# Kernel tuning notes

Hardware: AMD Instinct MI355X
Metric: run time of the kernel (lower is better)

Reference implementation:

```python
import jax, jax.numpy as jnp
import numpy as np

ANGULAR_WEIGHT = 0.1
EPS = 1e-07


def nine_d_to_rotmat(nine_d):
    # nine_d: [B, 9] -> special-orthogonal [B, 3, 3] via SVD Procrustes
    mats = nine_d.reshape(-1, 3, 3)
    u, s, vt = jnp.linalg.svd(mats)
    dets = jnp.linalg.det(jnp.matmul(u, vt))          # [B]
    sign = jnp.where(dets < 0, -1.0, 1.0)             # flip last column of u if det<0
    u = u.at[:, :, -1].multiply(sign[:, None])
    return jnp.matmul(u, vt)                          # [B, 3, 3], det=+1


def setup_inputs() -> dict:
    key = jax.random.key(0)
    k1, k2 = jax.random.split(key)
    B = 524288
    pred = jax.random.normal(k1, (B, 9), dtype=jnp.float32)
    target = jax.random.normal(k2, (B, 9), dtype=jnp.float32)
    return {"pred": pred, "target": target}


def reference(pred, target):
    pred = pred.astype(jnp.float32)
    target = target.astype(jnp.float32)
    pred_rot = nine_d_to_rotmat(pred)      # [B,3,3]
    target_rot = nine_d_to_rotmat(target)  # [B,3,3]

    # chordal loss: mean squared Frobenius norm of difference
    diff = pred_rot - target_rot
    chordal_loss = jnp.mean(jnp.sum(diff * diff, axis=(1, 2)))

    # angular distance in degrees (original recomputes SVDs; same math)
    relative = jnp.matmul(jnp.swapaxes(pred_rot, 1, 2), target_rot)
    traces = jnp.einsum('bii->b', relative)
    cos_theta = jnp.clip((traces - 1.0) / 2.0, -1.0 + EPS, 1.0 - EPS)
    angular = jnp.arccos(cos_theta) * (180.0 / np.pi)
    angular_loss = jnp.mean(angular)

    return chordal_loss + ANGULAR_WEIGHT * angular_loss
```

## Files before the change

kernel.cpp:

```cpp
#include <hip/hip_runtime.h>

#define ANGW 0.1f
#define CLIP_EPS 1e-7f
#define RAD2DEG 57.29577951308232f
#define PI_F 3.14159265358979f
#define PAIRS 4

__device__ __forceinline__ float frcp(float x)  { return __builtin_amdgcn_rcpf(x); }
__device__ __forceinline__ float frsq(float x)  { return __builtin_amdgcn_rsqf(x); }
__device__ __forceinline__ float fsqrt_(float x){ return __builtin_amdgcn_sqrtf(x); }

__device__ __forceinline__ float facos(float x) {
    float ax = fabsf(x);
    float p  = fmaf(ax, -0.0187293f, 0.0742610f);
    p        = fmaf(ax, p, -0.2121144f);
    p        = fmaf(ax, p,  1.5707288f);
    float r  = fsqrt_(fmaxf(1.0f - ax, 0.0f)) * p;
    return x >= 0.0f ? r : PI_F - r;
}

__device__ __forceinline__ void nearest_rot(const float m[9], float R[9]) {
    float a00 = m[0]*m[0] + m[3]*m[3] + m[6]*m[6];
    float a11 = m[1]*m[1] + m[4]*m[4] + m[7]*m[7];
    float a22 = m[2]*m[2] + m[5]*m[5] + m[8]*m[8];
    float a01 = m[0]*m[1] + m[3]*m[4] + m[6]*m[7];
    float a02 = m[0]*m[2] + m[3]*m[5] + m[6]*m[8];
    float a12 = m[1]*m[2] + m[4]*m[5] + m[7]*m[8];

    float q   = (a00 + a11 + a22) * (1.0f/3.0f);
    float b00 = a00 - q, b11 = a11 - q, b22 = a22 - q;
    float trB2 = b00*b00 + b11*b11 + b22*b22
               + 2.0f*(a01*a01 + a02*a02 + a12*a12);
    float p    = fsqrt_(fmaxf(trB2 * (1.0f/6.0f), 1e-35f));
    float invp = frcp(p);
    float detB = b00*(b11*b22 - a12*a12)
               - a01*(a01*b22 - a12*a02)
               + a02*(a01*a12 - b11*a02);
    float r = ((detB * invp) * invp) * invp * 0.5f;
    r = fminf(fmaxf(r, -1.0f), 1.0f);
    float phi = facos(r) * (1.0f/3.0f);
    float cph = __cosf(phi);
    float sph = fsqrt_(fmaxf(1.0f - cph*cph, 0.0f));
    float e0 = q + 2.0f*p*cph;
    float e2 = q + p*(-cph - 1.7320508075688772f*sph);
    float e1 = 3.0f*q - e0 - e2;

#define EIGVEC(lam, vx, vy, vz) {                                             \
    float c00 = a00 - (lam), c11 = a11 - (lam), c22 = a22 - (lam);            \
                                                                 \
    float x1 = c11*c22 - a12*a12;                                             \
    float y1 = a12*a02 - a01*c22;                                             \
    float z1 = a01*a12 - c11*a02;                                             \
                                                                 \
    float x2 = a01*c22 - a02*a12;                                             \
    float y2 = a02*a02 - c00*c22;                                             \
    float z2 = c00*a12 - a01*a02;                                             \
    float n1 = x1*x1 + y1*y1 + z1*z1;                                         \
    float n2 = x2*x2 + y2*y2 + z2*z2;                                         \
    bool s2  = n2 > n1;                                                       \
    float bx = s2 ? x2 : x1, by = s2 ? y2 : y1, bz = s2 ? z2 : z1;            \
    float bn = s2 ? n2 : n1;                                                  \
    float inv = frsq(fmaxf(bn, 1e-35f));                                      \
    vx = bx*inv; vy = by*inv; vz = bz*inv; }

    float v1x, v1y, v1z; EIGVEC(e0, v1x, v1y, v1z)
    float v2x, v2y, v2z; EIGVEC(e1, v2x, v2y, v2z)
#undef EIGVEC
    (void)e2;

    float v3x = v1y*v2z - v1z*v2y;
    float v3y = v1z*v2x - v1x*v2z;
    float v3z = v1x*v2y - v1y*v2x;

    float w1x = m[0]*v1x + m[1]*v1y + m[2]*v1z;
    float w1y = m[3]*v1x + m[4]*v1y + m[5]*v1z;
    float w1z = m[6]*v1x + m[7]*v1y + m[8]*v1z;
    float inv1 = frsq(fmaxf(w1x*w1x + w1y*w1y + w1z*w1z, 1e-35f));
    float u1x = w1x*inv1, u1y = w1y*inv1, u1z = w1z*inv1;

    float w2x = m[0]*v2x + m[1]*v2y + m[2]*v2z;
    float w2y = m[3]*v2x + m[4]*v2y + m[5]*v2z;
    float w2z = m[6]*v2x + m[7]*v2y + m[8]*v2z;
    float d = u1x*w2x + u1y*w2y + u1z*w2z;
    w2x = fmaf(-d, u1x, w2x); w2y = fmaf(-d, u1y, w2y); w2z = fmaf(-d, u1z, w2z);
    float inv2 = frsq(fmaxf(w2x*w2x + w2y*w2y + w2z*w2z, 1e-35f));
    float u2x = w2x*inv2, u2y = w2y*inv2, u2z = w2z*inv2;

    float u3x = u1y*u2z - u1z*u2y;
    float u3y = u1z*u2x - u1x*u2z;
    float u3z = u1x*u2y - u1y*u2x;

    R[0] = u1x*v1x + u2x*v2x + u3x*v3x;
    R[1] = u1x*v1y + u2x*v2y + u3x*v3y;
    R[2] = u1x*v1z + u2x*v2z + u3x*v3z;
    R[3] = u1y*v1x + u2y*v2x + u3y*v3x;
    R[4] = u1y*v1y + u2y*v2y + u3y*v3y;
    R[5] = u1y*v1z + u2y*v2z + u3y*v3z;
    R[6] = u1z*v1x + u2z*v2x + u3z*v3x;
    R[7] = u1z*v1y + u2z*v2y + u3z*v3y;
    R[8] = u1z*v1z + u2z*v2z + u3z*v3z;
}

__device__ __forceinline__ float pair_loss(const float mp[9], const float mt[9]) {
    float Rp[9], Rt[9];
    nearest_rot(mp, Rp);
    nearest_rot(mt, Rt);
    float tr = 0.0f;
#pragma unroll
    for (int k = 0; k < 9; ++k) tr = fmaf(Rp[k], Rt[k], tr);
    float ch = fmaf(-2.0f, tr, 6.0f);
    float cosd = (tr - 1.0f) * 0.5f;
    cosd = fminf(fmaxf(cosd, -1.0f + CLIP_EPS), 1.0f - CLIP_EPS);
    return ch + ANGW * (facos(cosd) * RAD2DEG);
}

__global__ __launch_bounds__(256) void rotloss_kernel(
    const float* __restrict__ pred, const float* __restrict__ target,
    float* __restrict__ out, int B, int T, float invB)
{
    const int t = blockIdx.x * 256 + threadIdx.x;

    float mp[PAIRS][9], mt[PAIRS][9];
    bool  valid[PAIRS];
#pragma unroll
    for (int k = 0; k < PAIRS; ++k) {
        const int i = t + k * T;
        valid[k] = i < B;
        if (valid[k]) {
            __builtin_memcpy(mp[k], pred   + (size_t)i * 9, 36);
            __builtin_memcpy(mt[k], target + (size_t)i * 9, 36);
        }
    }

    float loss = 0.0f;
#pragma unroll
    for (int k = 0; k < PAIRS; ++k)
        if (valid[k]) loss += pair_loss(mp[k], mt[k]);

#pragma unroll
    for (int off = 32; off > 0; off >>= 1) loss += __shfl_down(loss, off, 64);
    __shared__ float wsum[4];
    const int lane = threadIdx.x & 63, wv = threadIdx.x >> 6;
    if (lane == 0) wsum[wv] = loss;
    __syncthreads();
    if (threadIdx.x == 0) {
        atomicAdd(out, (wsum[0] + wsum[1] + wsum[2] + wsum[3]) * invB);
    }
}

extern "C" void kernel_launch(void* const* d_in, const int* in_sizes, int n_in,
                              void* d_out, int out_size, void* d_ws, size_t ws_size,
                              hipStream_t stream) {
    const float* pred   = (const float*)d_in[0];
    const float* target = (const float*)d_in[1];
    float* out = (float*)d_out;
    const int B = in_sizes[0] / 9;
    const float invB = 1.0f / (float)B;
    const int grid = (B + 256 * PAIRS - 1) / (256 * PAIRS);
    const int T = grid * 256;

    rotloss_kernel<<<grid, 256, 0, stream>>>(pred, target, out, B, T, invB);
}
```

Baseline: 86.58 us.

## Interleave eight matrix decompositions stage-by-stage for ILP, pad invalid rows with identity

Inlines the per-matrix SVD-free rotation routine into the kernel and restructures it so all eight matrices (four pred/target pairs) advance through each stage together: Gram entries, eigenvalues, eigenvectors, then U columns. This interleaving exposes independent instruction streams to hide latency of transcendental and dependent arithmetic. Invalid slots are filled with identity and masked at accumulation, which makes the compute branch-free. It also sets launch_bounds minimum blocks to 2. Keeping eight matrices' state live at once raises register pressure and may cause spills or lower occupancy.

```diff
diff --git a/kernel.cpp b/kernel.cpp
--- a/kernel.cpp
+++ b/kernel.cpp
@@ -5,6 +5,7 @@
 #define RAD2DEG 57.29577951308232f
 #define PI_F 3.14159265358979f
 #define PAIRS 4
+#define NR (2*PAIRS)
 
 __device__ __forceinline__ float frcp(float x)  { return __builtin_amdgcn_rcpf(x); }
 __device__ __forceinline__ float frsq(float x)  { return __builtin_amdgcn_rsqf(x); }
@@ -19,42 +20,72 @@
     return x >= 0.0f ? r : PI_F - r;
 }
 
-__device__ __forceinline__ void nearest_rot(const float m[9], float R[9]) {
-    float a00 = m[0]*m[0] + m[3]*m[3] + m[6]*m[6];
-    float a11 = m[1]*m[1] + m[4]*m[4] + m[7]*m[7];
-    float a22 = m[2]*m[2] + m[5]*m[5] + m[8]*m[8];
-    float a01 = m[0]*m[1] + m[3]*m[4] + m[6]*m[7];
-    float a02 = m[0]*m[2] + m[3]*m[5] + m[6]*m[8];
-    float a12 = m[1]*m[2] + m[4]*m[5] + m[7]*m[8];
+__global__ __launch_bounds__(256, 2) void rotloss_kernel(
+    const float* __restrict__ pred, const float* __restrict__ target,
+    float* __restrict__ out, int B, int T, float invB)
+{
+    const int t = blockIdx.x * 256 + threadIdx.x;
 
-    float q   = (a00 + a11 + a22) * (1.0f/3.0f);
-    float b00 = a00 - q, b11 = a11 - q, b22 = a22 - q;
-    float trB2 = b00*b00 + b11*b11 + b22*b22
-               + 2.0f*(a01*a01 + a02*a02 + a12*a12);
-    float p    = fsqrt_(fmaxf(trB2 * (1.0f/6.0f), 1e-35f));
-    float invp = frcp(p);
-    float detB = b00*(b11*b22 - a12*a12)
-               - a01*(a01*b22 - a12*a02)
-               + a02*(a01*a12 - b11*a02);
-    float r = ((detB * invp) * invp) * invp * 0.5f;
-    r = fminf(fmaxf(r, -1.0f), 1.0f);
-    float phi = facos(r) * (1.0f/3.0f);
-    float cph = __cosf(phi);
-    float sph = fsqrt_(fmaxf(1.0f - cph*cph, 0.0f));
-    float e0 = q + 2.0f*p*cph;
-    float e2 = q + p*(-cph - 1.7320508075688772f*sph);
-    float e1 = 3.0f*q - e0 - e2;
+    float m[NR][9];
+    bool  valid[PAIRS];
+#pragma unroll
+    for (int k = 0; k < PAIRS; ++k) {
+        const int i = t + k * T;
+        valid[k] = i < B;
+        if (valid[k]) {
+            __builtin_memcpy(m[2*k],     pred   + (size_t)i * 9, 36);
+            __builtin_memcpy(m[2*k + 1], target + (size_t)i * 9, 36);
+        } else {
+#pragma unroll
+            for (int j = 0; j < 9; ++j) {
+                m[2*k][j]     = (j == 0 || j == 4 || j == 8) ? 1.0f : 0.0f;
+                m[2*k + 1][j] = (j == 0 || j == 4 || j == 8) ? 1.0f : 0.0f;
+            }
+        }
+    }
 
-#define EIGVEC(lam, vx, vy, vz) {                                             \
-    float c00 = a00 - (lam), c11 = a11 - (lam), c22 = a22 - (lam);            \
-                                                                 \
-    float x1 = c11*c22 - a12*a12;                                             \
-    float y1 = a12*a02 - a01*c22;                                             \
-    float z1 = a01*a12 - c11*a02;                                             \
-                                                                 \
-    float x2 = a01*c22 - a02*a12;                                             \
-    float y2 = a02*a02 - c00*c22;                                             \
-    float z2 = c00*a12 - a01*a02;                                             \
+    float a00[NR], a11[NR], a22[NR], a01[NR], a02[NR], a12[NR];
+#pragma unroll
+    for (int r = 0; r < NR; ++r) {
+        a00[r] = m[r][0]*m[r][0] + m[r][3]*m[r][3] + m[r][6]*m[r][6];
+        a11[r] = m[r][1]*m[r][1] + m[r][4]*m[r][4] + m[r][7]*m[r][7];
+        a22[r] = m[r][2]*m[r][2] + m[r][5]*m[r][5] + m[r][8]*m[r][8];
+        a01[r] = m[r][0]*m[r][1] + m[r][3]*m[r][4] + m[r][6]*m[r][7];
+        a02[r] = m[r][0]*m[r][2] + m[r][3]*m[r][5] + m[r][6]*m[r][8];
+        a12[r] = m[r][1]*m[r][2] + m[r][4]*m[r][5] + m[r][7]*m[r][8];
+    }
+
+    float e0[NR], e1[NR];
+#pragma unroll
+    for (int r = 0; r < NR; ++r) {
+        float q   = (a00[r] + a11[r] + a22[r]) * (1.0f/3.0f);
+        float b00 = a00[r] - q, b11 = a11[r] - q, b22 = a22[r] - q;
+        float trB2 = b00*b00 + b11*b11 + b22*b22
+                   + 2.0f*(a01[r]*a01[r] + a02[r]*a02[r] + a12[r]*a12[r]);
+        float p    = fsqrt_(fmaxf(trB2 * (1.0f/6.0f), 1e-35f));
+        float invp = frcp(p);
+        float detB = b00*(b11*b22 - a12[r]*a12[r])
+                   - a01[r]*(a01[r]*b22 - a12[r]*a02[r])
+                   + a02[r]*(a01[r]*a12[r] - b11*a02[r]);
+        float rr = ((detB * invp) * invp) * invp * 0.5f;
+        rr = fminf(fmaxf(rr, -1.0f), 1.0f);
+        float phi = facos(rr) * (1.0f/3.0f);
+        float cph = __cosf(phi);
+        float sph = fsqrt_(fmaxf(1.0f - cph*cph, 0.0f));
+        e0[r] = q + 2.0f*p*cph;
+        float e2 = q + p*(-cph - 1.7320508075688772f*sph);
+        e1[r] = 3.0f*q - e0[r] - e2;
+    }
+
+    float v1x[NR], v1y[NR], v1z[NR], v2x[NR], v2y[NR], v2z[NR];
+#define EIGVEC(r, lam, vx, vy, vz) {                                          \
+    float c00 = a00[r] - (lam), c11 = a11[r] - (lam), c22 = a22[r] - (lam);   \
+    float x1 = c11*c22 - a12[r]*a12[r];                                       \
+    float y1 = a12[r]*a02[r] - a01[r]*c22;                                    \
+    float z1 = a01[r]*a12[r] - c11*a02[r];                                    \
+    float x2 = a01[r]*c22 - a02[r]*a12[r];                                    \
+    float y2 = a02[r]*a02[r] - c00*c22;                                       \
+    float z2 = c00*a12[r] - a01[r]*a02[r];                                    \
     float n1 = x1*x1 + y1*y1 + z1*z1;                                         \
     float n2 = x2*x2 + y2*y2 + z2*z2;                                         \
     bool s2  = n2 > n1;                                                       \
@@ -62,80 +93,70 @@
     float bn = s2 ? n2 : n1;                                                  \
     float inv = frsq(fmaxf(bn, 1e-35f));                                      \
     vx = bx*inv; vy = by*inv; vz = bz*inv; }
+#pragma unroll
+    for (int r = 0; r < NR; ++r) {
+        EIGVEC(r, e0[r], v1x[r], v1y[r], v1z[r])
+        EIGVEC(r, e1[r], v2x[r], v2y[r], v2z[r])
+    }
+#undef EIGVEC
 
-    float v1x, v1y, v1z; EIGVEC(e0, v1x, v1y, v1z)
-    float v2x, v2y, v2z; EIGVEC(e1, v2x, v2y, v2z)
-#undef EIGVEC
-    (void)e2;
+    float u1x[NR], u1y[NR], u1z[NR], u2x[NR], u2y[NR], u2z[NR];
+#pragma unroll
+    for (int r = 0; r < NR; ++r) {
+        float w1x = m[r][0]*v1x[r] + m[r][1]*v1y[r] + m[r][2]*v1z[r];
+        float w1y = m[r][3]*v1x[r] + m[r][4]*v1y[r] + m[r][5]*v1z[r];
+        float w1z = m[r][6]*v1x[r] + m[r][7]*v1y[r] + m[r][8]*v1z[r];
+        float inv1 = frsq(fmaxf(w1x*w1x + w1y*w1y + w1z*w1z, 1e-35f));
+        u1x[r] = w1x*inv1; u1y[r] = w1y*inv1; u1z[r] = w1z*inv1;
 
-    float v3x = v1y*v2z - v1z*v2y;
-    float v3y = v1z*v2x - v1x*v2z;
-    float v3z = v1x*v2y - v1y*v2x;
-
-    float w1x = m[0]*v1x + m[1]*v1y + m[2]*v1z;
-    float w1y = m[3]*v1x + m[4]*v1y + m[5]*v1z;
-    float w1z = m[6]*v1x + m[7]*v1y + m[8]*v1z;
-    float inv1 = frsq(fmaxf(w1x*w1x + w1y*w1y + w1z*w1z, 1e-35f));
-    float u1x = w1x*inv1, u1y = w1y*inv1, u1z = w1z*inv1;
-
-    float w2x = m[0]*v2x + m[1]*v2y + m[2]*v2z;
-    float w2y = m[3]*v2x + m[4]*v2y + m[5]*v2z;
-    float w2z = m[6]*v2x + m[7]*v2y + m[8]*v2z;
-    float d = u1x*w2x + u1y*w2y + u1z*w2z;
-    w2x = fmaf(-d, u1x, w2x); w2y = fmaf(-d, u1y, w2y); w2z = fmaf(-d, u1z, w2z);
-    float inv2 = frsq(fmaxf(w2x*w2x + w2y*w2y + w2z*w2z, 1e-35f));
-    float u2x = w2x*inv2, u2y = w2y*inv2, u2z = w2z*inv2;
-
-    float u3x = u1y*u2z - u1z*u2y;
-    float u3y = u1z*u2x - u1x*u2z;
-    float u3z = u1x*u2y - u1y*u2x;
-
-    R[0] = u1x*v1x + u2x*v2x + u3x*v3x;
-    R[1] = u1x*v1y + u2x*v2y + u3x*v3y;
-    R[2] = u1x*v1z + u2x*v2z + u3x*v3z;
-    R[3] = u1y*v1x + u2y*v2x + u3y*v3x;
-    R[4] = u1y*v1y + u2y*v2y + u3y*v3y;
-    R[5] = u1y*v1z + u2y*v2z + u3y*v3z;
-    R[6] = u1z*v1x + u2z*v2x + u3z*v3x;
-    R[7] = u1z*v1y + u2z*v2y + u3z*v3y;
-    R[8] = u1z*v1z + u2z*v2z + u3z*v3z;
-}
-
-__device__ __forceinline__ float pair_loss(const float mp[9], const float mt[9]) {
-    float Rp[9], Rt[9];
-    nearest_rot(mp, Rp);
-    nearest_rot(mt, Rt);
-    float tr = 0.0f;
-#pragma unroll
-    for (int k = 0; k < 9; ++k) tr = fmaf(Rp[k], Rt[k], tr);
-    float ch = fmaf(-2.0f, tr, 6.0f);
-    float cosd = (tr - 1.0f) * 0.5f;
-    cosd = fminf(fmaxf(cosd, -1.0f + CLIP_EPS), 1.0f - CLIP_EPS);
-    return ch + ANGW * (facos(cosd) * RAD2DEG);
-}
-
-__global__ __launch_bounds__(256) void rotloss_kernel(
-    const float* __restrict__ pred, const float* __restrict__ target,
-    float* __restrict__ out, int B, int T, float invB)
-{
-    const int t = blockIdx.x * 256 + threadIdx.x;
-
-    float mp[PAIRS][9], mt[PAIRS][9];
-    bool  valid[PAIRS];
-#pragma unroll
-    for (int k = 0; k < PAIRS; ++k) {
-        const int i = t + k * T;
-        valid[k] = i < B;
-        if (valid[k]) {
-            __builtin_memcpy(mp[k], pred   + (size_t)i * 9, 36);
-            __builtin_memcpy(mt[k], target + (size_t)i * 9, 36);
-        }
+        float w2x = m[r][0]*v2x[r] + m[r][1]*v2y[r] + m[r][2]*v2z[r];
+        float w2y = m[r][3]*v2x[r] + m[r][4]*v2y[r] + m[r][5]*v2z[r];
+        float w2z = m[r][6]*v2x[r] + m[r][7]*v2y[r] + m[r][8]*v2z[r];
+        float d = u1x[r]*w2x + u1y[r]*w2y + u1z[r]*w2z;
+        w2x = fmaf(-d, u1x[r], w2x); w2y = fmaf(-d, u1y[r], w2y); w2z = fmaf(-d, u1z[r], w2z);
+        float inv2 = frsq(fmaxf(w2x*w2x + w2y*w2y + w2z*w2z, 1e-35f));
+        u2x[r] = w2x*inv2; u2y[r] = w2y*inv2; u2z[r] = w2z*inv2;
     }
 
     float loss = 0.0f;
 #pragma unroll
-    for (int k = 0; k < PAIRS; ++k)
-        if (valid[k]) loss += pair_loss(mp[k], mt[k]);
+    for (int k = 0; k < PAIRS; ++k) {
+        const int rp = 2*k, rt = 2*k + 1;
+        float up[3][3] = {{u1x[rp],u1y[rp],u1z[rp]},
+                          {u2x[rp],u2y[rp],u2z[rp]},
+                          {u1y[rp]*u2z[rp]-u1z[rp]*u2y[rp],
+                           u1z[rp]*u2x[rp]-u1x[rp]*u2z[rp],
+                           u1x[rp]*u2y[rp]-u1y[rp]*u2x[rp]}};
+        float vp[3][3] = {{v1x[rp],v1y[rp],v1z[rp]},
+                          {v2x[rp],v2y[rp],v2z[rp]},
+                          {v1y[rp]*v2z[rp]-v1z[rp]*v2y[rp],
+                           v1z[rp]*v2x[rp]-v1x[rp]*v2z[rp],
+                           v1x[rp]*v2y[rp]-v1y[rp]*v2x[rp]}};
+        float ut[3][3] = {{u1x[rt],u1y[rt],u1z[rt]},
+                          {u2x[rt],u2y[rt],u2z[rt]},
+                          {u1y[rt]*u2z[rt]-u1z[rt]*u2y[rt],
+                           u1z[rt]*u2x[rt]-u1x[rt]*u2z[rt],
+                           u1x[rt]*u2y[rt]-u1y[rt]*u2x[rt]}};
+        float vt[3][3] = {{v1x[rt],v1y[rt],v1z[rt]},
+                          {v2x[rt],v2y[rt],v2z[rt]},
+                          {v1y[rt]*v2z[rt]-v1z[rt]*v2y[rt],
+                           v1z[rt]*v2x[rt]-v1x[rt]*v2z[rt],
+                           v1x[rt]*v2y[rt]-v1y[rt]*v2x[rt]}};
+        float trv = 0.0f;
+#pragma unroll
+        for (int i = 0; i < 3; ++i)
+#pragma unroll
+            for (int j = 0; j < 3; ++j) {
+                float rpij = up[0][i]*vp[0][j] + up[1][i]*vp[1][j] + up[2][i]*vp[2][j];
+                float rtij = ut[0][i]*vt[0][j] + ut[1][i]*vt[1][j] + ut[2][i]*vt[2][j];
+                trv = fmaf(rpij, rtij, trv);
+            }
+        float ch = fmaf(-2.0f, trv, 6.0f);
+        float cosd = (trv - 1.0f) * 0.5f;
+        cosd = fminf(fmaxf(cosd, -1.0f + CLIP_EPS), 1.0f - CLIP_EPS);
+        float pl = ch + ANGW * (facos(cosd) * RAD2DEG);
+        if (valid[k]) loss += pl;
+    }
 
 #pragma unroll
     for (int off = 32; off > 0; off >>= 1) loss += __shfl_down(loss, off, 64);
```

After: 85.74 us. No clear change (-1.0%).
